# Performance work log

Hardware: AMD Instinct MI355X
Metric: run time of the kernel (lower is better)

## Reference

```python
import jax, jax.numpy as jnp
import numpy as np

D_PAIR = 128
D_HIDDEN = 32
N_HEAD = 4
B, L = 1, 256
EPS = 1e-5


def setup_inputs() -> dict:
    key = jax.random.key(0)
    ks = jax.random.split(key, 9)
    dh = D_HIDDEN * N_HEAD  # 128
    s = 1.0 / np.sqrt(D_PAIR)
    return {
        'pair': jax.random.normal(ks[0], (B, L, L, D_PAIR), dtype=jnp.float32),
        'mask_2d': jnp.ones((B, L, L), dtype=bool),
        'ln_g': jnp.ones((D_PAIR,), dtype=jnp.float32),
        'ln_b': jnp.zeros((D_PAIR,), dtype=jnp.float32),
        'Wq': jax.random.normal(ks[1], (D_PAIR, dh), dtype=jnp.float32) * s,
        'Wk': jax.random.normal(ks[2], (D_PAIR, dh), dtype=jnp.float32) * s,
        'Wv': jax.random.normal(ks[3], (D_PAIR, dh), dtype=jnp.float32) * s,
        'Wb': jax.random.normal(ks[4], (D_PAIR, N_HEAD), dtype=jnp.float32) * s,
        'Wg': jax.random.normal(ks[5], (D_PAIR, N_HEAD), dtype=jnp.float32) * s,
        'Wo': jax.random.normal(ks[6], (dh, D_PAIR), dtype=jnp.float32) * s,
    }


def reference(pair, mask_2d, ln_g, ln_b, Wq, Wk, Wv, Wb, Wg, Wo):
    b, l = pair.shape[0], pair.shape[1]
    scaling = 1.0 / np.sqrt(D_HIDDEN)
    # LayerNorm over d_pair
    mu = jnp.mean(pair, axis=-1, keepdims=True)
    var = jnp.var(pair, axis=-1, keepdims=True)
    p = (pair - mu) * jax.lax.rsqrt(var + EPS) * ln_g + ln_b  # [B,L,L,C]

    q = (p @ Wq).reshape(b, l, l, N_HEAD, D_HIDDEN) * scaling
    k = (p @ Wk).reshape(b, l, l, N_HEAD, D_HIDDEN)
    v = (p @ Wv).reshape(b, l, l, N_HEAD, D_HIDDEN)
    bias = p @ Wb  # [B,L,L,H] indexed [b,j,k,h]

    # starting-node attention: logits[b,i,j,k,h]
    attn = jnp.einsum('bijhd,bikhd->bijkh', q, k) + bias[:, None]
    key_mask = jnp.any(mask_2d, axis=-1)  # [B,L] over k
    attn = jnp.where(key_mask[:, None, None, :, None], attn, -jnp.inf)
    attn = jax.nn.softmax(attn, axis=-2)
    out = jnp.einsum('bijkh,bikhd->bijhd', attn, v)

    gate = jax.nn.sigmoid(p @ Wg)[..., None]  # [B,L,L,H,1]
    out = gate * out
    out = out.reshape(b, l, l, N_HEAD * D_HIDDEN)
    return out @ Wo
```

## Files before the change

kernel.cpp:

```cpp
#include <hip/hip_runtime.h>
#include <hip/hip_bf16.h>
#include <stdint.h>

typedef __bf16 bf16_t;
typedef bf16_t bf16x8 __attribute__((ext_vector_type(8)));
typedef bf16_t bf16x4 __attribute__((ext_vector_type(4)));
typedef float f32x4 __attribute__((ext_vector_type(4)));
typedef uint32_t u32x4 __attribute__((ext_vector_type(4)));
typedef uint16_t u16x4 __attribute__((ext_vector_type(4)));

#define NROW 65536

__device__ __forceinline__ uint32_t swz(int rowkey, uint32_t byteoff) {
  return byteoff ^ (uint32_t)((rowkey & 7) << 4);
}

__device__ __forceinline__ uint32_t swzV(int d, uint32_t byteoff) {
  uint32_t key = (((uint32_t)d & 7u) ^ ((((uint32_t)d >> 3) & 3u) << 1)) & 7u;
  return byteoff ^ (key << 4);
}

__device__ __forceinline__ uint32_t pack_bf16_2(float lo, float hi) {
  uint16_t l = __builtin_bit_cast(uint16_t, (bf16_t)lo);
  uint16_t h = __builtin_bit_cast(uint16_t, (bf16_t)hi);
  return (uint32_t)l | ((uint32_t)h << 16);
}

__global__ void k0_prep(const float* __restrict__ Wq, const float* __restrict__ Wk,
                        const float* __restrict__ Wv, const float* __restrict__ Wb,
                        const float* __restrict__ Wg, const float* __restrict__ Wo,
                        bf16_t* __restrict__ wqt, bf16_t* __restrict__ wkt,
                        bf16_t* __restrict__ wvt, bf16_t* __restrict__ wot,
                        bf16_t* __restrict__ wbgt) {
  int idx = blockIdx.x * 256 + threadIdx.x;
  if (idx < 16384) {
    int r = idx >> 7, cc = idx & 127;
    const float qscale = 0.17677669529663687f;
    wqt[cc * 128 + r] = (bf16_t)(Wq[idx] * qscale);
    wkt[cc * 128 + r] = (bf16_t)(Wk[idx]);
    wvt[cc * 128 + r] = (bf16_t)(Wv[idx]);
    wot[cc * 128 + r] = (bf16_t)(Wo[idx]);
  }
  if (idx < 2048) {
    int cc = idx >> 7, r = idx & 127;
    float v = 0.0f;
    if (cc < 4) v = Wb[r * 4 + cc];
    else if (cc < 8) v = Wg[r * 4 + (cc - 4)];
    wbgt[cc * 128 + r] = (bf16_t)v;
  }
}

__global__ void k1_ln(const float* __restrict__ pair, const float* __restrict__ lng,
                      const float* __restrict__ lnb, bf16_t* __restrict__ pbuf) {
  int gw = (blockIdx.x * blockDim.x + threadIdx.x) >> 6;
  int lane = threadIdx.x & 63;
  int nw = (gridDim.x * blockDim.x) >> 6;
  float2 gg = *(const float2*)(lng + lane * 2);
  float2 bb = *(const float2*)(lnb + lane * 2);
  for (int row = gw; row < NROW; row += nw) {
    const float* src = pair + (size_t)row * 128;
    float2 x = *(const float2*)(src + lane * 2);
    float s = x.x + x.y, s2 = x.x * x.x + x.y * x.y;
#pragma unroll
    for (int m = 1; m < 64; m <<= 1) {
      s += __shfl_xor(s, m, 64);
      s2 += __shfl_xor(s2, m, 64);
    }
    float mu = s * (1.0f / 128.0f);
    float var = s2 * (1.0f / 128.0f) - mu * mu;
    float rs = rsqrtf(var + 1e-5f);
    float y0 = (x.x - mu) * rs * gg.x + bb.x;
    float y1 = (x.y - mu) * rs * gg.y + bb.y;
    *(uint32_t*)((char*)(pbuf + (size_t)row * 128) + lane * 4) = pack_bf16_2(y0, y1);
  }
}

__global__ __launch_bounds__(256) void k2_gemm(
    const bf16_t* __restrict__ pbuf, const bf16_t* __restrict__ wqt,
    const bf16_t* __restrict__ wbgt, bf16_t* __restrict__ qbuf,
    bf16_t* __restrict__ kbuf, bf16_t* __restrict__ vbuf,
    bf16_t* __restrict__ biasb, float* __restrict__ gatep) {
  __shared__ __align__(16) char smem[65536];
  const int y = blockIdx.y;
  const int m0 = blockIdx.x * 128;
  const int tid = threadIdx.x;
#pragma unroll
  for (int it = 0; it < 8; ++it) {
    int chunk = it * 256 + tid;
    int row = chunk >> 4, seg = chunk & 15;
    uint4 v = *(const uint4*)((const char*)pbuf + (size_t)(m0 + row) * 256 + seg * 16);
    *(uint4*)(smem + swz(row, row * 256 + seg * 16)) = v;
  }
  if (y < 3) {
    const bf16_t* w = wqt + y * 16384;
#pragma unroll
    for (int it = 0; it < 8; ++it) {
      int chunk = it * 256 + tid;
      int row = chunk >> 4, seg = chunk & 15;
      uint4 v = *(const uint4*)((const char*)w + row * 256 + seg * 16);
      *(uint4*)(smem + 32768 + swz(row, row * 256 + seg * 16)) = v;
    }
  } else {
    int row = tid >> 4, seg = tid & 15;
    uint4 v = *(const uint4*)((const char*)wbgt + row * 256 + seg * 16);
    *(uint4*)(smem + 32768 + swz(row, row * 256 + seg * 16)) = v;
  }
  __syncthreads();
  const int wid = tid >> 6, lane = tid & 63, g = lane >> 4, c = lane & 15;
  if (y < 3) {
    const int wr = wid >> 1, wc = wid & 1;
    f32x4 acc[4][4] = {};
#pragma unroll
    for (int ks = 0; ks < 4; ++ks) {
      bf16x8 a[4], bb[4];
#pragma unroll
      for (int mi = 0; mi < 4; ++mi) {
        int row = wr * 64 + mi * 16 + c;
        a[mi] = *(const bf16x8*)(smem + swz(row, row * 256 + ks * 64 + g * 16));
      }
#pragma unroll
      for (int ni = 0; ni < 4; ++ni) {
        int row = wc * 64 + ni * 16 + c;
        bb[ni] = *(const bf16x8*)(smem + 32768 + swz(row, row * 256 + ks * 64 + g * 16));
      }
#pragma unroll
      for (int mi = 0; mi < 4; ++mi)
#pragma unroll
        for (int ni = 0; ni < 4; ++ni)
          acc[mi][ni] = __builtin_amdgcn_mfma_f32_16x16x32_bf16(a[mi], bb[ni], acc[mi][ni], 0, 0, 0);
    }
    bf16_t* dst = (y == 0) ? qbuf : (y == 1) ? kbuf : vbuf;
#pragma unroll
    for (int mi = 0; mi < 4; ++mi)
#pragma unroll
      for (int ni = 0; ni < 4; ++ni)
#pragma unroll
        for (int r = 0; r < 4; ++r) {
          int row = m0 + wr * 64 + mi * 16 + g * 4 + r;
          int col = wc * 64 + ni * 16 + c;
          dst[(size_t)row * 128 + col] = (bf16_t)acc[mi][ni][r];
        }
  } else {
    f32x4 acc[2] = {};
#pragma unroll
    for (int ks = 0; ks < 4; ++ks) {
      int r0 = wid * 32 + c, r1 = r0 + 16;
      bf16x8 a0 = *(const bf16x8*)(smem + swz(r0, r0 * 256 + ks * 64 + g * 16));
      bf16x8 a1 = *(const bf16x8*)(smem + swz(r1, r1 * 256 + ks * 64 + g * 16));
      bf16x8 bb = *(const bf16x8*)(smem + 32768 + swz(c, c * 256 + ks * 64 + g * 16));
      acc[0] = __builtin_amdgcn_mfma_f32_16x16x32_bf16(a0, bb, acc[0], 0, 0, 0);
      acc[1] = __builtin_amdgcn_mfma_f32_16x16x32_bf16(a1, bb, acc[1], 0, 0, 0);
    }
#pragma unroll
    for (int mi = 0; mi < 2; ++mi)
#pragma unroll
      for (int r = 0; r < 4; ++r) {
        int row = m0 + wid * 32 + mi * 16 + g * 4 + r;
        float v = acc[mi][r];
        if (c < 4) biasb[(size_t)c * NROW + row] = (bf16_t)v;
        else if (c < 8) gatep[(size_t)(c - 4) * NROW + row] = 1.0f / (1.0f + __expf(-v));
      }
  }
}

__global__ __launch_bounds__(256, 2) void k3_attn(
    const bf16_t* __restrict__ qbuf, const bf16_t* __restrict__ kbuf,
    const bf16_t* __restrict__ vbuf, const bf16_t* __restrict__ biasb,
    const float* __restrict__ gatep, bf16_t* __restrict__ obuf) {
  __shared__ __align__(16) char smem[65536];
  const int ic = blockIdx.x, jq = blockIdx.y, h = blockIdx.z;
  const int tid = threadIdx.x, wid = tid >> 6, lane = tid & 63, g = lane >> 4, c = lane & 15;
  const char* bsrcg = (const char*)(biasb + (size_t)h * NROW + (size_t)jq * 64 * 256);
#pragma unroll
  for (int it = 0; it < 8; ++it) {
    int chunk = it * 256 + tid;
    int jl = chunk >> 5, seg = chunk & 31;
    u32x4 v = *(const u32x4*)(bsrcg + jl * 512 + seg * 16);
    *(u32x4*)(smem + swz(jl, jl * 512 + seg * 16)) = v;
  }
  const float* gateh = gatep + (size_t)h * NROW;
  const int jl = wid * 16 + c;
  const int jrow = jq * 64 + jl;
  for (int ii = 0; ii < 8; ++ii) {
    int i = ic * 8 + ii;
    const size_t base = ((size_t)i * 256) * 128 + h * 32;
    __syncthreads();
#pragma unroll
    for (int it = 0; it < 4; ++it) {
      int chunk = it * 256 + tid;
      int row = chunk >> 2, seg = chunk & 3;
      u32x4 kv = *(const u32x4*)((const char*)(kbuf + base + (size_t)row * 128) + seg * 16);
      u32x4 vv = *(const u32x4*)((const char*)(vbuf + base + (size_t)row * 128) + seg * 16);
      *(u32x4*)(smem + 32768 + swz(row, row * 64 + seg * 16)) = kv;
      const uint16_t* ve = (const uint16_t*)&vv;
#pragma unroll
      for (int e = 0; e < 8; ++e) {
        int d = seg * 8 + e;
        *(uint16_t*)(smem + 49152 + swzV(d, d * 512 + row * 2)) = ve[e];
      }
    }
    bf16x8 qf = __builtin_nontemporal_load(
        (const bf16x8*)((const char*)qbuf + ((size_t)(i * 256 + jrow) * 128 + h * 32) * 2 + g * 16));
    float gv0 = __builtin_nontemporal_load(gateh + (size_t)i * 256 + jrow);
    __syncthreads();
    f32x4 s[16];
#pragma unroll
    for (int kt = 0; kt < 16; ++kt) {
      bf16x4 b4 = *(const bf16x4*)(smem + swz(jl, jl * 512 + (kt * 16 + 4 * g) * 2));
      s[kt][0] = (float)b4[0];
      s[kt][1] = (float)b4[1];
      s[kt][2] = (float)b4[2];
      s[kt][3] = (float)b4[3];
    }
#pragma unroll
    for (int kt = 0; kt < 16; ++kt) {
      int krow = kt * 16 + c;
      bf16x8 kf = *(const bf16x8*)(smem + 32768 + swz(krow, krow * 64 + g * 16));
      s[kt] = __builtin_amdgcn_mfma_f32_16x16x32_bf16(kf, qf, s[kt], 0, 0, 0);
    }
    float sum = 0.0f;
#pragma unroll
    for (int kt = 0; kt < 16; ++kt)
#pragma unroll
      for (int r = 0; r < 4; ++r) {
        float e = __expf(s[kt][r]);
        s[kt][r] = e;
        sum += e;
      }
    sum += __shfl_xor(sum, 16, 64);
    sum += __shfl_xor(sum, 32, 64);
    __syncthreads();
    char* plds = smem + 32768 + wid * 4096;
    f32x4 o[2] = {};
#pragma unroll
    for (int q = 0; q < 4; ++q) {
#pragma unroll
      for (int t = 0; t < 4; ++t) {
        int kt = q * 4 + t;
        int kkb = (t * 16 + 4 * g) * 2;
        uint2 pw;
        pw.x = pack_bf16_2(s[kt][0], s[kt][1]);
        pw.y = pack_bf16_2(s[kt][2], s[kt][3]);
        *(uint2*)(plds + swz(c, c * 128 + kkb)) = pw;
      }
#pragma unroll
      for (int t2 = 0; t2 < 2; ++t2) {
        int s8 = q * 2 + t2;
        bf16x8 pb = *(const bf16x8*)(plds + swz(c, c * 128 + t2 * 64 + g * 16));
        int d0 = c, d1 = 16 + c;
        bf16x8 va0 = *(const bf16x8*)(smem + 49152 + swzV(d0, d0 * 512 + s8 * 64 + g * 16));
        bf16x8 va1 = *(const bf16x8*)(smem + 49152 + swzV(d1, d1 * 512 + s8 * 64 + g * 16));
        o[0] = __builtin_amdgcn_mfma_f32_16x16x32_bf16(va0, pb, o[0], 0, 0, 0);
        o[1] = __builtin_amdgcn_mfma_f32_16x16x32_bf16(va1, pb, o[1], 0, 0, 0);
      }
    }
    float gv = gv0 / sum;
#pragma unroll
    for (int dt = 0; dt < 2; ++dt) {
      u16x4 w;
      uint32_t lo = pack_bf16_2(o[dt][0] * gv, o[dt][1] * gv);
      uint32_t hi = pack_bf16_2(o[dt][2] * gv, o[dt][3] * gv);
      w[0] = (uint16_t)(lo & 0xffff);
      w[1] = (uint16_t)(lo >> 16);
      w[2] = (uint16_t)(hi & 0xffff);
      w[3] = (uint16_t)(hi >> 16);
      __builtin_nontemporal_store(
          w, (u16x4*)((char*)(obuf + base + (size_t)jrow * 128) + (dt * 16 + 4 * g) * 2));
    }
  }
}

__global__ __launch_bounds__(256) void k4_out(const bf16_t* __restrict__ obuf,
                                              const bf16_t* __restrict__ wot,
                                              float* __restrict__ out) {
  __shared__ __align__(16) char smem[65536];
  const int m0 = blockIdx.x * 128;
  const int tid = threadIdx.x;
#pragma unroll
  for (int it = 0; it < 8; ++it) {
    int chunk = it * 256 + tid;
    int row = chunk >> 4, seg = chunk & 15;
    uint4 v = *(const uint4*)((const char*)obuf + (size_t)(m0 + row) * 256 + seg * 16);
    *(uint4*)(smem + swz(row, row * 256 + seg * 16)) = v;
    uint4 w = *(const uint4*)((const char*)wot + row * 256 + seg * 16);
    *(uint4*)(smem + 32768 + swz(row, row * 256 + seg * 16)) = w;
  }
  __syncthreads();
  const int wid = tid >> 6, lane = tid & 63, g = lane >> 4, c = lane & 15;
  const int wr = wid >> 1, wc = wid & 1;
  f32x4 acc[4][4] = {};
#pragma unroll
  for (int ks = 0; ks < 4; ++ks) {
    bf16x8 a[4], bb[4];
#pragma unroll
    for (int mi = 0; mi < 4; ++mi) {
      int row = wr * 64 + mi * 16 + c;
      a[mi] = *(const bf16x8*)(smem + swz(row, row * 256 + ks * 64 + g * 16));
    }
#pragma unroll
    for (int ni = 0; ni < 4; ++ni) {
      int row = wc * 64 + ni * 16 + c;
      bb[ni] = *(const bf16x8*)(smem + 32768 + swz(row, row * 256 + ks * 64 + g * 16));
    }
#pragma unroll
    for (int mi = 0; mi < 4; ++mi)
#pragma unroll
      for (int ni = 0; ni < 4; ++ni)
        acc[mi][ni] = __builtin_amdgcn_mfma_f32_16x16x32_bf16(a[mi], bb[ni], acc[mi][ni], 0, 0, 0);
  }
#pragma unroll
  for (int mi = 0; mi < 4; ++mi)
#pragma unroll
    for (int ni = 0; ni < 4; ++ni)
#pragma unroll
      for (int r = 0; r < 4; ++r) {
        int row = m0 + wr * 64 + mi * 16 + g * 4 + r;
        int col = wc * 64 + ni * 16 + c;
        out[(size_t)row * 128 + col] = acc[mi][ni][r];
      }
}

extern "C" void kernel_launch(void* const* d_in, const int* in_sizes, int n_in,
                              void* d_out, int out_size, void* d_ws, size_t ws_size,
                              hipStream_t stream) {
  const float* pair = (const float*)d_in[0];
  const float* lng = (const float*)d_in[2];
  const float* lnb = (const float*)d_in[3];
  const float* Wq = (const float*)d_in[4];
  const float* Wk = (const float*)d_in[5];
  const float* Wv = (const float*)d_in[6];
  const float* Wb = (const float*)d_in[7];
  const float* Wg = (const float*)d_in[8];
  const float* Wo = (const float*)d_in[9];

  char* ws = (char*)d_ws;
  bf16_t* biasb = (bf16_t*)(ws + 0);
  float* gatep = (float*)(ws + 524288);
  bf16_t* wqt = (bf16_t*)(ws + 1572864);
  bf16_t* wot = (bf16_t*)(ws + 1671168);
  bf16_t* wbgt = (bf16_t*)(ws + 1703936);
  bf16_t* pbuf = (bf16_t*)(ws + 1708032);
  bf16_t* qbuf = (bf16_t*)(ws + 18485248);
  bf16_t* kbuf = (bf16_t*)(ws + 35262464);
  bf16_t* vbuf = (bf16_t*)(ws + 52039680);
  bf16_t* obuf = pbuf;

  bf16_t* wkt = wqt + 16384;
  bf16_t* wvt = wqt + 32768;

  k0_prep<<<64, 256, 0, stream>>>(Wq, Wk, Wv, Wb, Wg, Wo, wqt, wkt, wvt, wot, wbgt);
  k1_ln<<<512, 256, 0, stream>>>(pair, lng, lnb, pbuf);
  k2_gemm<<<dim3(512, 4), 256, 0, stream>>>(pbuf, wqt, wbgt, qbuf, kbuf, vbuf, biasb, gatep);
  k3_attn<<<dim3(32, 4, 4), 256, 0, stream>>>(qbuf, kbuf, vbuf, biasb, gatep, obuf);
  k4_out<<<512, 256, 0, stream>>>(obuf, wot, (float*)d_out);
}
```

Baseline: 98.30 us.

## Reuse loaded pair tile across all projections and prefetch next K/V in attention

The projection GEMM now loads each 128-row tile of the normalized pair activations once and loops over the Q, K, V and bias/gate weight sets inside one block, instead of launching four blocks that each reload the same tile. The attention kernel register-prefetches the next i-slice's K, V, Q fragment and gate value while computing the current one, so global load latency is overlapped with MFMA work. Costs are fewer blocks in the GEMM grid (less parallelism), extra barriers, and higher register pressure in the attention kernel, which is launched with two blocks per CU and could spill or lose occupancy.

```diff
diff --git a/kernel.cpp b/kernel.cpp
--- a/kernel.cpp
+++ b/kernel.cpp
@@ -81,7 +81,6 @@
     bf16_t* __restrict__ kbuf, bf16_t* __restrict__ vbuf,
     bf16_t* __restrict__ biasb, float* __restrict__ gatep) {
   __shared__ __align__(16) char smem[65536];
-  const int y = blockIdx.y;
   const int m0 = blockIdx.x * 128;
   const int tid = threadIdx.x;
 #pragma unroll
@@ -91,7 +90,10 @@
     uint4 v = *(const uint4*)((const char*)pbuf + (size_t)(m0 + row) * 256 + seg * 16);
     *(uint4*)(smem + swz(row, row * 256 + seg * 16)) = v;
   }
-  if (y < 3) {
+  const int wid = tid >> 6, lane = tid & 63, g = lane >> 4, c = lane & 15;
+  const int wr = wid >> 1, wc = wid & 1;
+  for (int y = 0; y < 3; ++y) {
+    __syncthreads();
     const bf16_t* w = wqt + y * 16384;
 #pragma unroll
     for (int it = 0; it < 8; ++it) {
@@ -100,15 +102,7 @@
       uint4 v = *(const uint4*)((const char*)w + row * 256 + seg * 16);
       *(uint4*)(smem + 32768 + swz(row, row * 256 + seg * 16)) = v;
     }
-  } else {
-    int row = tid >> 4, seg = tid & 15;
-    uint4 v = *(const uint4*)((const char*)wbgt + row * 256 + seg * 16);
-    *(uint4*)(smem + 32768 + swz(row, row * 256 + seg * 16)) = v;
-  }
-  __syncthreads();
-  const int wid = tid >> 6, lane = tid & 63, g = lane >> 4, c = lane & 15;
-  if (y < 3) {
-    const int wr = wid >> 1, wc = wid & 1;
+    __syncthreads();
     f32x4 acc[4][4] = {};
 #pragma unroll
     for (int ks = 0; ks < 4; ++ks) {
@@ -140,7 +134,15 @@
           int col = wc * 64 + ni * 16 + c;
           dst[(size_t)row * 128 + col] = (bf16_t)acc[mi][ni][r];
         }
-  } else {
+  }
+  __syncthreads();
+  {
+    int row = tid >> 4, seg = tid & 15;
+    uint4 v = *(const uint4*)((const char*)wbgt + row * 256 + seg * 16);
+    *(uint4*)(smem + 32768 + swz(row, row * 256 + seg * 16)) = v;
+  }
+  __syncthreads();
+  {
     f32x4 acc[2] = {};
 #pragma unroll
     for (int ks = 0; ks < 4; ++ks) {
@@ -174,13 +176,30 @@
 #pragma unroll
   for (int it = 0; it < 8; ++it) {
     int chunk = it * 256 + tid;
-    int jl = chunk >> 5, seg = chunk & 31;
-    u32x4 v = *(const u32x4*)(bsrcg + jl * 512 + seg * 16);
-    *(u32x4*)(smem + swz(jl, jl * 512 + seg * 16)) = v;
+    int jl2 = chunk >> 5, seg = chunk & 31;
+    u32x4 v = *(const u32x4*)(bsrcg + jl2 * 512 + seg * 16);
+    *(u32x4*)(smem + swz(jl2, jl2 * 512 + seg * 16)) = v;
   }
   const float* gateh = gatep + (size_t)h * NROW;
   const int jl = wid * 16 + c;
   const int jrow = jq * 64 + jl;
+  u32x4 kr[4], vr[4], kr2[4], vr2[4];
+  bf16x8 qf, qf2;
+  float gv0, gv2;
+  {
+    int i0 = ic * 8;
+    const size_t base0 = ((size_t)i0 * 256) * 128 + h * 32;
+#pragma unroll
+    for (int it = 0; it < 4; ++it) {
+      int chunk = it * 256 + tid;
+      int row = chunk >> 2, seg = chunk & 3;
+      kr[it] = *(const u32x4*)((const char*)(kbuf + base0 + (size_t)row * 128) + seg * 16);
+      vr[it] = *(const u32x4*)((const char*)(vbuf + base0 + (size_t)row * 128) + seg * 16);
+    }
+    qf = __builtin_nontemporal_load(
+        (const bf16x8*)((const char*)qbuf + ((size_t)(i0 * 256 + jrow) * 128 + h * 32) * 2 + g * 16));
+    gv0 = __builtin_nontemporal_load(gateh + (size_t)i0 * 256 + jrow);
+  }
   for (int ii = 0; ii < 8; ++ii) {
     int i = ic * 8 + ii;
     const size_t base = ((size_t)i * 256) * 128 + h * 32;
@@ -189,19 +208,27 @@
     for (int it = 0; it < 4; ++it) {
       int chunk = it * 256 + tid;
       int row = chunk >> 2, seg = chunk & 3;
-      u32x4 kv = *(const u32x4*)((const char*)(kbuf + base + (size_t)row * 128) + seg * 16);
-      u32x4 vv = *(const u32x4*)((const char*)(vbuf + base + (size_t)row * 128) + seg * 16);
-      *(u32x4*)(smem + 32768 + swz(row, row * 64 + seg * 16)) = kv;
-      const uint16_t* ve = (const uint16_t*)&vv;
+      *(u32x4*)(smem + 32768 + swz(row, row * 64 + seg * 16)) = kr[it];
+      const uint16_t* ve = (const uint16_t*)&vr[it];
 #pragma unroll
       for (int e = 0; e < 8; ++e) {
         int d = seg * 8 + e;
         *(uint16_t*)(smem + 49152 + swzV(d, d * 512 + row * 2)) = ve[e];
       }
     }
-    bf16x8 qf = __builtin_nontemporal_load(
-        (const bf16x8*)((const char*)qbuf + ((size_t)(i * 256 + jrow) * 128 + h * 32) * 2 + g * 16));
-    float gv0 = __builtin_nontemporal_load(gateh + (size_t)i * 256 + jrow);
+    if (ii < 7) {
+      const size_t basen = base + 32768;
+#pragma unroll
+      for (int it = 0; it < 4; ++it) {
+        int chunk = it * 256 + tid;
+        int row = chunk >> 2, seg = chunk & 3;
+        kr2[it] = *(const u32x4*)((const char*)(kbuf + basen + (size_t)row * 128) + seg * 16);
+        vr2[it] = *(const u32x4*)((const char*)(vbuf + basen + (size_t)row * 128) + seg * 16);
+      }
+      qf2 = __builtin_nontemporal_load(
+          (const bf16x8*)((const char*)qbuf + ((size_t)((i + 1) * 256 + jrow) * 128 + h * 32) * 2 + g * 16));
+      gv2 = __builtin_nontemporal_load(gateh + (size_t)(i + 1) * 256 + jrow);
+    }
     __syncthreads();
     f32x4 s[16];
 #pragma unroll
@@ -267,6 +294,13 @@
       __builtin_nontemporal_store(
           w, (u16x4*)((char*)(obuf + base + (size_t)jrow * 128) + (dt * 16 + 4 * g) * 2));
     }
+#pragma unroll
+    for (int it = 0; it < 4; ++it) {
+      kr[it] = kr2[it];
+      vr[it] = vr2[it];
+    }
+    qf = qf2;
+    gv0 = gv2;
   }
 }
 
@@ -350,7 +384,7 @@
 
   k0_prep<<<64, 256, 0, stream>>>(Wq, Wk, Wv, Wb, Wg, Wo, wqt, wkt, wvt, wot, wbgt);
   k1_ln<<<512, 256, 0, stream>>>(pair, lng, lnb, pbuf);
-  k2_gemm<<<dim3(512, 4), 256, 0, stream>>>(pbuf, wqt, wbgt, qbuf, kbuf, vbuf, biasb, gatep);
+  k2_gemm<<<512, 256, 0, stream>>>(pbuf, wqt, wbgt, qbuf, kbuf, vbuf, biasb, gatep);
   k3_attn<<<dim3(32, 4, 4), 256, 0, stream>>>(qbuf, kbuf, vbuf, biasb, gatep, obuf);
   k4_out<<<512, 256, 0, stream>>>(obuf, wot, (float*)d_out);
 }
```

New measurement: 102.0 us. 3.7% more time.

## Reuse LN tile across projections in GEMM and keep bias in registers in attention

Applied to the files above, without the earlier changes.

The projection GEMM now loads each 128-row tile of the normalized pair once and loops over the Q, K, V and bias/gate weights inside one block, instead of launching four blocks that each reload the same tile. In the attention kernel, each lane holds its bias row in registers instead of staging it in shared memory. This halves LDS use to 32KB, allows three blocks per CU, and doubles the grid so each block handles 4 rows instead of 8. The trade-offs are fewer, longer GEMM blocks with extra barriers, and more bias reloads plus register pressure in attention.

```diff
diff --git a/kernel.cpp b/kernel.cpp
--- a/kernel.cpp
+++ b/kernel.cpp
@@ -81,7 +81,6 @@
     bf16_t* __restrict__ kbuf, bf16_t* __restrict__ vbuf,
     bf16_t* __restrict__ biasb, float* __restrict__ gatep) {
   __shared__ __align__(16) char smem[65536];
-  const int y = blockIdx.y;
   const int m0 = blockIdx.x * 128;
   const int tid = threadIdx.x;
 #pragma unroll
@@ -91,7 +90,10 @@
     uint4 v = *(const uint4*)((const char*)pbuf + (size_t)(m0 + row) * 256 + seg * 16);
     *(uint4*)(smem + swz(row, row * 256 + seg * 16)) = v;
   }
-  if (y < 3) {
+  const int wid = tid >> 6, lane = tid & 63, g = lane >> 4, c = lane & 15;
+  const int wr = wid >> 1, wc = wid & 1;
+  for (int y = 0; y < 3; ++y) {
+    __syncthreads();
     const bf16_t* w = wqt + y * 16384;
 #pragma unroll
     for (int it = 0; it < 8; ++it) {
@@ -100,15 +102,7 @@
       uint4 v = *(const uint4*)((const char*)w + row * 256 + seg * 16);
       *(uint4*)(smem + 32768 + swz(row, row * 256 + seg * 16)) = v;
     }
-  } else {
-    int row = tid >> 4, seg = tid & 15;
-    uint4 v = *(const uint4*)((const char*)wbgt + row * 256 + seg * 16);
-    *(uint4*)(smem + 32768 + swz(row, row * 256 + seg * 16)) = v;
-  }
-  __syncthreads();
-  const int wid = tid >> 6, lane = tid & 63, g = lane >> 4, c = lane & 15;
-  if (y < 3) {
-    const int wr = wid >> 1, wc = wid & 1;
+    __syncthreads();
     f32x4 acc[4][4] = {};
 #pragma unroll
     for (int ks = 0; ks < 4; ++ks) {
@@ -140,7 +134,15 @@
           int col = wc * 64 + ni * 16 + c;
           dst[(size_t)row * 128 + col] = (bf16_t)acc[mi][ni][r];
         }
-  } else {
+  }
+  __syncthreads();
+  {
+    int row = tid >> 4, seg = tid & 15;
+    uint4 v = *(const uint4*)((const char*)wbgt + row * 256 + seg * 16);
+    *(uint4*)(smem + 32768 + swz(row, row * 256 + seg * 16)) = v;
+  }
+  __syncthreads();
+  {
     f32x4 acc[2] = {};
 #pragma unroll
     for (int ks = 0; ks < 4; ++ks) {
@@ -163,26 +165,23 @@
   }
 }
 
-__global__ __launch_bounds__(256, 2) void k3_attn(
+__global__ __launch_bounds__(256, 3) void k3_attn(
     const bf16_t* __restrict__ qbuf, const bf16_t* __restrict__ kbuf,
     const bf16_t* __restrict__ vbuf, const bf16_t* __restrict__ biasb,
     const float* __restrict__ gatep, bf16_t* __restrict__ obuf) {
-  __shared__ __align__(16) char smem[65536];
+  __shared__ __align__(16) char smem[32768];
   const int ic = blockIdx.x, jq = blockIdx.y, h = blockIdx.z;
   const int tid = threadIdx.x, wid = tid >> 6, lane = tid & 63, g = lane >> 4, c = lane & 15;
-  const char* bsrcg = (const char*)(biasb + (size_t)h * NROW + (size_t)jq * 64 * 256);
-#pragma unroll
-  for (int it = 0; it < 8; ++it) {
-    int chunk = it * 256 + tid;
-    int jl = chunk >> 5, seg = chunk & 31;
-    u32x4 v = *(const u32x4*)(bsrcg + jl * 512 + seg * 16);
-    *(u32x4*)(smem + swz(jl, jl * 512 + seg * 16)) = v;
-  }
-  const float* gateh = gatep + (size_t)h * NROW;
   const int jl = wid * 16 + c;
   const int jrow = jq * 64 + jl;
-  for (int ii = 0; ii < 8; ++ii) {
-    int i = ic * 8 + ii;
+  uint2 bj[16];
+  const char* bsrc = (const char*)(biasb + (size_t)h * NROW + (size_t)jrow * 256);
+#pragma unroll
+  for (int kt = 0; kt < 16; ++kt)
+    bj[kt] = *(const uint2*)(bsrc + kt * 32 + 8 * g);
+  const float* gateh = gatep + (size_t)h * NROW;
+  for (int ii = 0; ii < 4; ++ii) {
+    int i = ic * 4 + ii;
     const size_t base = ((size_t)i * 256) * 128 + h * 32;
     __syncthreads();
 #pragma unroll
@@ -191,12 +190,12 @@
       int row = chunk >> 2, seg = chunk & 3;
       u32x4 kv = *(const u32x4*)((const char*)(kbuf + base + (size_t)row * 128) + seg * 16);
       u32x4 vv = *(const u32x4*)((const char*)(vbuf + base + (size_t)row * 128) + seg * 16);
-      *(u32x4*)(smem + 32768 + swz(row, row * 64 + seg * 16)) = kv;
+      *(u32x4*)(smem + swz(row, row * 64 + seg * 16)) = kv;
       const uint16_t* ve = (const uint16_t*)&vv;
 #pragma unroll
       for (int e = 0; e < 8; ++e) {
         int d = seg * 8 + e;
-        *(uint16_t*)(smem + 49152 + swzV(d, d * 512 + row * 2)) = ve[e];
+        *(uint16_t*)(smem + 16384 + swzV(d, d * 512 + row * 2)) = ve[e];
       }
     }
     bf16x8 qf = __builtin_nontemporal_load(
@@ -206,7 +205,7 @@
     f32x4 s[16];
 #pragma unroll
     for (int kt = 0; kt < 16; ++kt) {
-      bf16x4 b4 = *(const bf16x4*)(smem + swz(jl, jl * 512 + (kt * 16 + 4 * g) * 2));
+      bf16x4 b4 = __builtin_bit_cast(bf16x4, bj[kt]);
       s[kt][0] = (float)b4[0];
       s[kt][1] = (float)b4[1];
       s[kt][2] = (float)b4[2];
@@ -215,7 +214,7 @@
 #pragma unroll
     for (int kt = 0; kt < 16; ++kt) {
       int krow = kt * 16 + c;
-      bf16x8 kf = *(const bf16x8*)(smem + 32768 + swz(krow, krow * 64 + g * 16));
+      bf16x8 kf = *(const bf16x8*)(smem + swz(krow, krow * 64 + g * 16));
       s[kt] = __builtin_amdgcn_mfma_f32_16x16x32_bf16(kf, qf, s[kt], 0, 0, 0);
     }
     float sum = 0.0f;
@@ -230,7 +229,7 @@
     sum += __shfl_xor(sum, 16, 64);
     sum += __shfl_xor(sum, 32, 64);
     __syncthreads();
-    char* plds = smem + 32768 + wid * 4096;
+    char* plds = smem + wid * 4096;
     f32x4 o[2] = {};
 #pragma unroll
     for (int q = 0; q < 4; ++q) {
@@ -248,8 +247,8 @@
         int s8 = q * 2 + t2;
         bf16x8 pb = *(const bf16x8*)(plds + swz(c, c * 128 + t2 * 64 + g * 16));
         int d0 = c, d1 = 16 + c;
-        bf16x8 va0 = *(const bf16x8*)(smem + 49152 + swzV(d0, d0 * 512 + s8 * 64 + g * 16));
-        bf16x8 va1 = *(const bf16x8*)(smem + 49152 + swzV(d1, d1 * 512 + s8 * 64 + g * 16));
+        bf16x8 va0 = *(const bf16x8*)(smem + 16384 + swzV(d0, d0 * 512 + s8 * 64 + g * 16));
+        bf16x8 va1 = *(const bf16x8*)(smem + 16384 + swzV(d1, d1 * 512 + s8 * 64 + g * 16));
         o[0] = __builtin_amdgcn_mfma_f32_16x16x32_bf16(va0, pb, o[0], 0, 0, 0);
         o[1] = __builtin_amdgcn_mfma_f32_16x16x32_bf16(va1, pb, o[1], 0, 0, 0);
       }
@@ -350,7 +349,7 @@
 
   k0_prep<<<64, 256, 0, stream>>>(Wq, Wk, Wv, Wb, Wg, Wo, wqt, wkt, wvt, wot, wbgt);
   k1_ln<<<512, 256, 0, stream>>>(pair, lng, lnb, pbuf);
-  k2_gemm<<<dim3(512, 4), 256, 0, stream>>>(pbuf, wqt, wbgt, qbuf, kbuf, vbuf, biasb, gatep);
-  k3_attn<<<dim3(32, 4, 4), 256, 0, stream>>>(qbuf, kbuf, vbuf, biasb, gatep, obuf);
+  k2_gemm<<<512, 256, 0, stream>>>(pbuf, wqt, wbgt, qbuf, kbuf, vbuf, biasb, gatep);
+  k3_attn<<<dim3(64, 4, 4), 256, 0, stream>>>(qbuf, kbuf, vbuf, biasb, gatep, obuf);
   k4_out<<<512, 256, 0, stream>>>(obuf, wot, (float*)d_out);
 }
```

Result: slower. 224.5 us (+128.4%).
